# Performance work log

Measured on AMD Instinct MI355X. Metric: run time of the kernel, lower is better.

## Reference

```python
import jax, jax.numpy as jnp
import numpy as np

N_NODES = 100000
N_HEDGES = 30000
N_PINS = 400000
D = 128          # hidden_channels
H = 4            # heads
K = D // H       # per-head dim
N_BLOCKS = 4     # n_layers=2, each layer = (vertex2edge, edge2vertex)
LN_EPS = 1e-5


def setup_inputs() -> dict:
    key = jax.random.key(0)
    ks = jax.random.split(key, 10)
    s = 1.0 / np.sqrt(D)
    return {
        "x_0": jax.random.normal(ks[0], (N_NODES, D), jnp.float32),
        "Kw": jax.random.normal(ks[1], (N_BLOCKS, H, D, K), jnp.float32) * s,
        "Vw": jax.random.normal(ks[2], (N_BLOCKS, H, D, K), jnp.float32) * s,
        "Qw": jax.random.normal(ks[3], (N_BLOCKS, H, K), jnp.float32) * s,
        "W1": jax.random.normal(ks[4], (N_BLOCKS, D, D), jnp.float32) * s,
        "b1": jnp.zeros((N_BLOCKS, D), jnp.float32),
        "W2": jax.random.normal(ks[5], (N_BLOCKS, D, D), jnp.float32) * s,
        "b2": jnp.zeros((N_BLOCKS, D), jnp.float32),
        "ln0_g": jnp.ones((N_BLOCKS, D), jnp.float32),
        "ln0_b": jnp.zeros((N_BLOCKS, D), jnp.float32),
        "ln1_g": jnp.ones((N_BLOCKS, D), jnp.float32),
        "ln1_b": jnp.zeros((N_BLOCKS, D), jnp.float32),
        "node_idx": jax.random.randint(ks[6], (N_PINS,), 0, N_NODES),
        "hedge_idx": jax.random.randint(ks[7], (N_PINS,), 0, N_HEDGES),
        "n_hyperedges": N_HEDGES,
    }


def _ln(x, g, b):
    mu = jnp.mean(x, -1, keepdims=True)
    var = jnp.mean((x - mu) ** 2, -1, keepdims=True)
    return (x - mu) * jax.lax.rsqrt(var + LN_EPS) * g + b


def _segment_softmax(logits, seg, num_segments):
    # softmax over incident pins grouped by target (sparse softmax over source dim)
    m = jax.ops.segment_max(logits, seg, num_segments=num_segments)
    ex = jnp.exp(logits - m[seg])
    denom = jax.ops.segment_sum(ex, seg, num_segments=num_segments)
    return ex / denom[seg]


def _block(x_src, src, tgt, n_tgt, Kw, Vw, Qw, W1, b1, W2, b2, g0, be0, g1, be1):
    # Multi-head PMA attention with a single learned query per head.
    Kx = jnp.einsum('nd,hdk->nhk', x_src, Kw)           # [n_src, H, K]
    Vx = jnp.einsum('nd,hdk->nhk', x_src, Vw)           # [n_src, H, K]
    logits = jnp.einsum('hk,nhk->nh', Qw, Kx)           # [n_src, H]
    w = _segment_softmax(logits[src], tgt, n_tgt)       # [E, H]
    msg = (w[:, :, None] * Vx[src]).reshape(-1, H * K)  # [E, D] head-concat
    agg = jax.ops.segment_sum(msg, tgt, num_segments=n_tgt)  # [n_tgt, D]
    x = _ln(agg + Qw.reshape(1, H * K), g0, be0)        # Q skip + LN0
    h = jnp.maximum(x @ W1 + b1, 0.0) @ W2 + b2         # 2-layer MLP
    return _ln(x + h, g1, be1)                          # residual + LN1


def reference(x_0, Kw, Vw, Qw, W1, b1, W2, b2, ln0_g, ln0_b, ln1_g, ln1_b,
              node_idx, hedge_idx, n_hyperedges):
    n_nodes = x_0.shape[0]
    x0, x1 = x_0, None
    for layer in range(N_BLOCKS // 2):
        bv, bev = 2 * layer, 2 * layer + 1
        # vertex -> hyperedge
        x1 = jax.nn.relu(_block(x0, node_idx, hedge_idx, n_hyperedges,
                                Kw[bv], Vw[bv], Qw[bv], W1[bv], b1[bv], W2[bv], b2[bv],
                                ln0_g[bv], ln0_b[bv], ln1_g[bv], ln1_b[bv]))
        # hyperedge -> vertex
        x0 = jax.nn.relu(_block(x1, hedge_idx, node_idx, n_nodes,
                                Kw[bev], Vw[bev], Qw[bev], W1[bev], b1[bev], W2[bev], b2[bev],
                                ln0_g[bev], ln0_b[bev], ln1_g[bev], ln1_b[bev]))
    return (x0, x1)
```

## Files before the change

### kernel.cpp

```cpp
#include <hip/hip_runtime.h>

#define N_NODES 100000
#define N_HEDGES 30000
#define N_PINS 400000
#define NPN 100096
#define NPH 30080
#define OVF_CAP 8192
#define SCAN_BH 118
#define SCAN_BN 391

typedef __attribute__((ext_vector_type(8))) short bf16x8;
typedef __attribute__((ext_vector_type(4))) float f32x4;
typedef unsigned short ushort_t;

__device__ __forceinline__ unsigned short f2bf(float f) {
  unsigned int u = __float_as_uint(f);
  u += 0x7FFF + ((u >> 16) & 1);
  return (unsigned short)(u >> 16);
}
__device__ __forceinline__ float bf2f(unsigned short s) {
  return __uint_as_float(((unsigned int)s) << 16);
}
__device__ __forceinline__ void gload16(const void* g, void* l) {
  __builtin_amdgcn_global_load_lds(
      (const __attribute__((address_space(1))) unsigned int*)g,
      (__attribute__((address_space(3))) unsigned int*)l, 16, 0, 0);
}

__global__ __launch_bounds__(256) void fused_front(
    const float* __restrict__ x0_in, ushort_t* __restrict__ x0b,
    const int* __restrict__ node_idx, const int* __restrict__ hedge_idx,
    int* __restrict__ cntN, int* __restrict__ cntH, unsigned* __restrict__ rank2,
    const float* __restrict__ Kw, const float* __restrict__ Vw,
    const float* __restrict__ Qw, const float* __restrict__ W1,
    const float* __restrict__ W2, ushort_t* __restrict__ Vvqsw,
    ushort_t* __restrict__ W1sw, ushort_t* __restrict__ W2sw) {
  int gsz = gridDim.x * 256;
  int tid = blockIdx.x * 256 + threadIdx.x;
  int rn = 0, rh = 0;
  bool hasPin = tid < N_PINS;
  if (hasPin) {
    int n_i = node_idx[tid], h_i = hedge_idx[tid];
    rn = atomicAdd(&cntN[n_i], 1);
    rh = atomicAdd(&cntH[h_i], 1);
  }
  for (int i = tid; i < N_NODES * 16; i += gsz) {
    const float4* s = (const float4*)x0_in + (size_t)i * 2;
    float4 a = s[0], b = s[1];
    uint4 o;
    o.x = ((unsigned)f2bf(a.y) << 16) | f2bf(a.x);
    o.y = ((unsigned)f2bf(a.w) << 16) | f2bf(a.z);
    o.z = ((unsigned)f2bf(b.y) << 16) | f2bf(b.x);
    o.w = ((unsigned)f2bf(b.w) << 16) | f2bf(b.z);
    ((uint4*)x0b)[i] = o;
  }
  for (int i = tid; i < 4 * 144 * 128; i += gsz) {
    int b = i / 18432, r = i % 18432, c = r >> 7, d = r & 127;
    float v;
    if (c < 128) {
      v = Vw[((b * 4 + (c >> 5)) * 128 + d) * 32 + (c & 31)];
    } else if (c < 132) {
      int h = c - 128;
      const float* kp = Kw + ((b * 4 + h) * 128 + d) * 32;
      const float* qp = Qw + (b * 4 + h) * 32;
      float s = 0.f;
      for (int k = 0; k < 32; ++k) s += kp[k] * qp[k];
      v = s;
    } else {
      v = 0.f;
    }
    int L = (c * 256 + d * 2) ^ ((c & 7) << 4);
    Vvqsw[b * 18432 + L / 2] = f2bf(v);
  }
  for (int i = tid; i < 4 * 128 * 128; i += gsz) {
    int b = i >> 14, r = i & 16383, c = r >> 7, k = r & 127;
    int L = (c * 256 + k * 2) ^ ((c & 7) << 4);
    int idx = b * 16384 + L / 2;
    W1sw[idx] = f2bf(W1[b * 16384 + k * 128 + c]);
    W2sw[idx] = f2bf(W2[b * 16384 + k * 128 + c]);
  }
  if (hasPin) rank2[tid] = ((unsigned)rh << 16) | (unsigned)rn;
}

__global__ __launch_bounds__(256) void csr_scan2(
    const int* __restrict__ cntH, int2* __restrict__ segH, int* __restrict__ ovfH,
    const int* __restrict__ cntN, int2* __restrict__ segN, int* __restrict__ ovfN,
    int* __restrict__ gctr) {
  __shared__ int wsum[4];
  __shared__ int bbase;
  bool isH = (int)blockIdx.x < SCAN_BH;
  const int* cnt = isH ? cntH : cntN;
  int2* seg = isH ? segH : segN;
  int* ovf = isH ? ovfH : ovfN;
  int* g = gctr + (isH ? 0 : 1);
  int* oc = gctr + (isH ? 2 : 3);
  int thresh = isH ? 32 : 16;
  int n = isH ? N_HEDGES : N_NODES;
  int i = (isH ? (int)blockIdx.x : (int)blockIdx.x - SCAN_BH) * 256 + threadIdx.x;
  int lane = threadIdx.x & 63, wid = threadIdx.x >> 6;
  int v = (i < n) ? cnt[i] : 0;
  int sc = v;
#pragma unroll
  for (int s = 1; s < 64; s <<= 1) {
    int tv = __shfl_up(sc, s);
    if (lane >= s) sc += tv;
  }
  if (lane == 63) wsum[wid] = sc;
  __syncthreads();
  if (threadIdx.x == 0) {
    int s0 = wsum[0], s1 = wsum[1], s2 = wsum[2], s3 = wsum[3];
    wsum[0] = 0; wsum[1] = s0; wsum[2] = s0 + s1; wsum[3] = s0 + s1 + s2;
    bbase = atomicAdd(g, s0 + s1 + s2 + s3);
  }
  __syncthreads();
  if (i < n) {
    int st = bbase + wsum[wid] + (sc - v);
    seg[i] = make_int2(st, v);
    if (v > thresh) {
      int k = atomicAdd(oc, 1);
      if (k < OVF_CAP) ovf[k] = i;
    }
  }
}

__global__ __launch_bounds__(256) void csr_fill(
    const int* __restrict__ node_idx, const int* __restrict__ hedge_idx,
    const unsigned* __restrict__ rank2, const int2* __restrict__ segN,
    const int2* __restrict__ segH, int* __restrict__ pinsN,
    int* __restrict__ pinsH) {
  int e = blockIdx.x * 256 + threadIdx.x;
  if (e < N_PINS) {
    int n = node_idx[e], h = hedge_idx[e];
    unsigned r2 = rank2[e];
    pinsH[segH[h].x + (int)(r2 >> 16)] = n;
    pinsN[segN[n].x + (int)(r2 & 0xffffu)] = h;
  }
}

__global__ __launch_bounds__(256) void transform_k(
    const ushort_t* __restrict__ xb, const ushort_t* __restrict__ Bsw,
    ushort_t* __restrict__ Vxb, float* __restrict__ lg, int n) {
  __shared__ char Blds[36864];
  __shared__ char Olds[16384];
  int t = threadIdx.x, l = t & 63, w = t >> 6;
  size_t r0 = (size_t)blockIdx.x * 64;
#pragma unroll
  for (int it = 0; it < 9; ++it) {
    int off = it * 4096 + w * 1024 + l * 16;
    gload16((const char*)Bsw + off, Blds + off);
  }
  __syncthreads();

  f32x4 acc[9];
#pragma unroll
  for (int ct = 0; ct < 9; ++ct) acc[ct] = (f32x4){0.f, 0.f, 0.f, 0.f};
  int swz = (l & 7) << 4;
  int lbase = (l & 15) * 256 + (l >> 4) * 16;
  const ushort_t* abase = xb + (r0 + w * 16 + (l & 15)) * 128 + (l >> 4) * 8;
#pragma unroll
  for (int kk = 0; kk < 4; ++kk) {
    bf16x8 a = *(const bf16x8*)(abase + kk * 32);
#pragma unroll
    for (int ct = 0; ct < 9; ++ct) {
      bf16x8 b = *(const bf16x8*)(Blds + ((ct * 4096 + kk * 64 + lbase) ^ swz));
      acc[ct] = __builtin_amdgcn_mfma_f32_16x16x32_bf16(a, b, acc[ct], 0, 0, 0);
    }
  }
  if ((l & 15) < 4) {
    size_t rb = r0 + w * 16 + (l >> 4) * 4;
#pragma unroll
    for (int j = 0; j < 4; ++j) lg[(rb + j) * 4 + (l & 15)] = acc[8][j];
  }
  int row64 = w * 16 + (l >> 4) * 4;
#pragma unroll
  for (int ct = 0; ct < 8; ++ct) {
    int c2 = (ct * 16 + (l & 15)) * 2;
#pragma unroll
    for (int j = 0; j < 4; ++j) {
      int r = row64 + j;
      int addr = (r * 256 + c2) ^ ((r & 0xC) << 3);
      *(ushort_t*)(Olds + addr) = f2bf(acc[ct][j]);
    }
  }
  __syncthreads();
#pragma unroll
  for (int it = 0; it < 4; ++it) {
    int L = it * 4096 + t * 16;
    int r = L >> 8;
    int phys = L ^ ((r & 0xC) << 3);
    *(uint4*)((char*)Vxb + r0 * 256 + L) = *(const uint4*)(Olds + phys);
  }
}

template <int L>
__global__ __launch_bounds__(256) void attn_g(
    const ushort_t* __restrict__ Vxb, const float* __restrict__ lg,
    const int2* __restrict__ seg, const int* __restrict__ pins,
    const float* __restrict__ Qflat, const float* __restrict__ g0,
    const float* __restrict__ be0, ushort_t* __restrict__ xmidb, int n_tgt,
    int mainBlocks, const int* __restrict__ ovf, const int* __restrict__ ovfcnt) {
  constexpr int G = 64 / L;
  constexpr int C = 128 / L;
  __shared__ float wl[4][G][L][4];
  __shared__ int pl[4][G][L];
  int wid = threadIdx.x >> 6, lane = threadIdx.x & 63;
  const char* vb = (const char*)Vxb;

  if ((int)blockIdx.x < mainBlocks) {
    int g = lane / L, li = lane % L;
    int tg = ((int)blockIdx.x * 4 + wid) * G + g;
    bool tval = tg < n_tgt;
    int2 sc = tval ? seg[tg] : make_int2(0, 0);
    int base = sc.x, deg = sc.y;
    bool fast = deg <= L;
    int mydeg = (tval && fast) ? deg : 0;
    bool act = li < mydeg;
    int p = act ? pins[base + li] : 0;
    float4 l4;
    if (act) l4 = *(const float4*)(lg + p * 4);
    else l4 = make_float4(-3.4e38f, -3.4e38f, -3.4e38f, -3.4e38f);
    float m0 = l4.x, m1 = l4.y, m2 = l4.z, m3 = l4.w;
#pragma unroll
    for (int off = 1; off < L; off <<= 1) {
      m0 = fmaxf(m0, __shfl_xor(m0, off));
      m1 = fmaxf(m1, __shfl_xor(m1, off));
      m2 = fmaxf(m2, __shfl_xor(m2, off));
      m3 = fmaxf(m3, __shfl_xor(m3, off));
    }
    float e0 = __expf(l4.x - m0), e1 = __expf(l4.y - m1);
    float e2 = __expf(l4.z - m2), e3 = __expf(l4.w - m3);
    float s0 = e0, s1 = e1, s2 = e2, s3 = e3;
#pragma unroll
    for (int off = 1; off < L; off <<= 1) {
      s0 += __shfl_xor(s0, off);
      s1 += __shfl_xor(s1, off);
      s2 += __shfl_xor(s2, off);
      s3 += __shfl_xor(s3, off);
    }
    wl[wid][g][li][0] = e0 / s0;
    wl[wid][g][li][1] = e1 / s1;
    wl[wid][g][li][2] = e2 / s2;
    wl[wid][g][li][3] = e3 / s3;
    pl[wid][g][li] = p << 8;

    int myh = li / (L / 4);
    float acc[C];
#pragma unroll
    for (int c = 0; c < C; ++c) acc[c] = 0.f;
    for (int e = 0; e < mydeg; ++e) {
      int off = pl[wid][g][e];
      float wgt = wl[wid][g][e][myh];
      const char* src = vb + off + li * (C * 2);
      unsigned u[C / 2];
      if constexpr (C == 8) {
        uint4 v = *(const uint4*)src;
        u[0] = v.x; u[1] = v.y; u[2] = v.z; u[3] = v.w;
      } else {
        uint2 v = *(const uint2*)src;
        u[0] = v.x; u[1] = v.y;
      }
#pragma unroll
      for (int j = 0; j < C / 2; ++j) {
        acc[2 * j] = fmaf(wgt, __uint_as_float(u[j] << 16), acc[2 * j]);
        acc[2 * j + 1] = fmaf(wgt, __uint_as_float(u[j] & 0xffff0000u), acc[2 * j + 1]);
      }
    }
    float q[C], gv[C], bv[C];
#pragma unroll
    for (int j = 0; j < C / 4; ++j) {
      float4 t = *(const float4*)(Qflat + li * C + j * 4);
      q[j * 4] = t.x; q[j * 4 + 1] = t.y; q[j * 4 + 2] = t.z; q[j * 4 + 3] = t.w;
      t = *(const float4*)(g0 + li * C + j * 4);
      gv[j * 4] = t.x; gv[j * 4 + 1] = t.y; gv[j * 4 + 2] = t.z; gv[j * 4 + 3] = t.w;
      t = *(const float4*)(be0 + li * C + j * 4);
      bv[j * 4] = t.x; bv[j * 4 + 1] = t.y; bv[j * 4 + 2] = t.z; bv[j * 4 + 3] = t.w;
    }
    float t1 = 0.f, t2 = 0.f;
#pragma unroll
    for (int c = 0; c < C; ++c) {
      float x = acc[c] + q[c];
      acc[c] = x;
      t1 += x;
      t2 += x * x;
    }
#pragma unroll
    for (int off = 1; off < L; off <<= 1) {
      t1 += __shfl_xor(t1, off);
      t2 += __shfl_xor(t2, off);
    }
    float mean = t1 * (1.f / 128.f);
    float var = t2 * (1.f / 128.f) - mean * mean;
    float rs = rsqrtf(var + 1e-5f);
    if (tval && fast) {
      float o[C];
#pragma unroll
      for (int c = 0; c < C; ++c) o[c] = (acc[c] - mean) * rs * gv[c] + bv[c];
      char* dst = (char*)xmidb + (size_t)tg * 256 + li * (C * 2);
      if constexpr (C == 8) {
        uint4 pk;
        pk.x = ((unsigned)f2bf(o[1]) << 16) | f2bf(o[0]);
        pk.y = ((unsigned)f2bf(o[3]) << 16) | f2bf(o[2]);
        pk.z = ((unsigned)f2bf(o[5]) << 16) | f2bf(o[4]);
        pk.w = ((unsigned)f2bf(o[7]) << 16) | f2bf(o[6]);
        *(uint4*)dst = pk;
      } else {
        uint2 pk;
        pk.x = ((unsigned)f2bf(o[1]) << 16) | f2bf(o[0]);
        pk.y = ((unsigned)f2bf(o[3]) << 16) | f2bf(o[2]);
        *(uint2*)dst = pk;
      }
    }
    return;
  }

  int cnt = *ovfcnt;
  if (cnt > OVF_CAP) cnt = OVF_CAP;
  int head = lane >> 4;
  for (int idx = ((int)blockIdx.x - mainBlocks) * 4 + wid; idx < cnt; idx += 128) {
    int tg = ovf[idx];
    int2 sc = seg[tg];
    int base = sc.x, deg = sc.y;
    float m0 = -3.4e38f, m1 = -3.4e38f, m2 = -3.4e38f, m3 = -3.4e38f;
    for (int i = lane; i < deg; i += 64) {
      int p = pins[base + i];
      float4 l4 = *(const float4*)(lg + p * 4);
      m0 = fmaxf(m0, l4.x); m1 = fmaxf(m1, l4.y);
      m2 = fmaxf(m2, l4.z); m3 = fmaxf(m3, l4.w);
    }
#pragma unroll
    for (int off = 1; off < 64; off <<= 1) {
      m0 = fmaxf(m0, __shfl_xor(m0, off));
      m1 = fmaxf(m1, __shfl_xor(m1, off));
      m2 = fmaxf(m2, __shfl_xor(m2, off));
      m3 = fmaxf(m3, __shfl_xor(m3, off));
    }
    float s0 = 0.f, s1 = 0.f, s2 = 0.f, s3 = 0.f;
    for (int i = lane; i < deg; i += 64) {
      int p = pins[base + i];
      float4 l4 = *(const float4*)(lg + p * 4);
      s0 += __expf(l4.x - m0); s1 += __expf(l4.y - m1);
      s2 += __expf(l4.z - m2); s3 += __expf(l4.w - m3);
    }
#pragma unroll
    for (int off = 1; off < 64; off <<= 1) {
      s0 += __shfl_xor(s0, off);
      s1 += __shfl_xor(s1, off);
      s2 += __shfl_xor(s2, off);
      s3 += __shfl_xor(s3, off);
    }
    float mh = (head & 2) ? ((head & 1) ? m3 : m2) : ((head & 1) ? m1 : m0);
    float sh = (head & 2) ? ((head & 1) ? s3 : s2) : ((head & 1) ? s1 : s0);
    float rdh = (deg > 0) ? 1.f / sh : 0.f;
    float acc0 = 0.f, acc1 = 0.f;
    for (int e = 0; e < deg; ++e) {
      int p = pins[base + e];
      float w0 = __expf(lg[p * 4 + head] - mh) * rdh;
      unsigned int v = *(const unsigned int*)(vb + (p << 8) + lane * 4);
      acc0 = fmaf(w0, __uint_as_float(v << 16), acc0);
      acc1 = fmaf(w0, __uint_as_float(v & 0xffff0000u), acc1);
    }
    float2 q2 = ((const float2*)Qflat)[lane];
    float x0v = acc0 + q2.x;
    float x1v = acc1 + q2.y;
    float t1 = x0v + x1v, t2 = x0v * x0v + x1v * x1v;
#pragma unroll
    for (int off = 1; off < 64; off <<= 1) {
      t1 += __shfl_xor(t1, off);
      t2 += __shfl_xor(t2, off);
    }
    float mean = t1 * (1.f / 128.f);
    float var = t2 * (1.f / 128.f) - mean * mean;
    float rs = rsqrtf(var + 1e-5f);
    float2 gg = ((const float2*)g0)[lane];
    float2 bb = ((const float2*)be0)[lane];
    float o0 = (x0v - mean) * rs * gg.x + bb.x;
    float o1 = (x1v - mean) * rs * gg.y + bb.y;
    unsigned int pk = ((unsigned int)f2bf(o1) << 16) | f2bf(o0);
    ((unsigned int*)xmidb)[tg * 64 + lane] = pk;
  }
}

__global__ __launch_bounds__(256) void mlp_k(
    const ushort_t* __restrict__ xmb, const ushort_t* __restrict__ W1sw,
    const float* __restrict__ b1, const ushort_t* __restrict__ W2sw,
    const float* __restrict__ b2, const float* __restrict__ g1,
    const float* __restrict__ be1, float* __restrict__ outf,
    ushort_t* __restrict__ outb, int n, int flags) {
  __shared__ char Wlds[32768];
  __shared__ char Hlds[16384];
  int t = threadIdx.x, l = t & 63, w = t >> 6;
  size_t r0 = (size_t)blockIdx.x * 64;
#pragma unroll
  for (int it = 0; it < 8; ++it) {
    int off = it * 4096 + w * 1024 + l * 16;
    gload16((const char*)W1sw + off, Wlds + off);
  }
  float b1v[8], b2v[8], g1v[8], be1v[8];
#pragma unroll
  for (int ct = 0; ct < 8; ++ct) {
    int c = ct * 16 + (l & 15);
    b1v[ct] = b1[c]; b2v[ct] = b2[c]; g1v[ct] = g1[c]; be1v[ct] = be1[c];
  }
  __syncthreads();

  int swz = (l & 7) << 4;
  int lbase = (l & 15) * 256 + (l >> 4) * 16;
  f32x4 acc[8];
#pragma unroll
  for (int ct = 0; ct < 8; ++ct) acc[ct] = (f32x4){b1v[ct], b1v[ct], b1v[ct], b1v[ct]};
  const ushort_t* abase = xmb + (r0 + w * 16 + (l & 15)) * 128 + (l >> 4) * 8;
#pragma unroll
  for (int kk = 0; kk < 4; ++kk) {
    bf16x8 a = *(const bf16x8*)(abase + kk * 32);
#pragma unroll
    for (int ct = 0; ct < 8; ++ct) {
      bf16x8 b = *(const bf16x8*)(Wlds + ((ct * 4096 + kk * 64 + lbase) ^ swz));
      acc[ct] = __builtin_amdgcn_mfma_f32_16x16x32_bf16(a, b, acc[ct], 0, 0, 0);
    }
  }
  int hbase = w * 4096;
#pragma unroll
  for (int ct = 0; ct < 8; ++ct) {
    int c2 = (ct * 16 + (l & 15)) * 2;
#pragma unroll
    for (int j = 0; j < 4; ++j) {
      int rl = (l >> 4) * 4 + j;
      int addr = hbase + ((rl * 256 + c2) ^ ((rl & 7) << 4));
      *(ushort_t*)(Hlds + addr) = f2bf(fmaxf(acc[ct][j], 0.f));
    }
  }
  __syncthreads();
#pragma unroll
  for (int it = 0; it < 8; ++it) {
    int off = it * 4096 + w * 1024 + l * 16;
    gload16((const char*)W2sw + off, Wlds + off);
  }
  __syncthreads();

  f32x4 acc2[8];
#pragma unroll
  for (int ct = 0; ct < 8; ++ct) acc2[ct] = (f32x4){b2v[ct], b2v[ct], b2v[ct], b2v[ct]};
#pragma unroll
  for (int kk = 0; kk < 4; ++kk) {
    bf16x8 a = *(const bf16x8*)(Hlds + (hbase + ((lbase + kk * 64) ^ swz)));
#pragma unroll
    for (int ct = 0; ct < 8; ++ct) {
      bf16x8 b = *(const bf16x8*)(Wlds + ((ct * 4096 + kk * 64 + lbase) ^ swz));
      acc2[ct] = __builtin_amdgcn_mfma_f32_16x16x32_bf16(a, b, acc2[ct], 0, 0, 0);
    }
  }
  size_t rbase = r0 + w * 16 + (l >> 4) * 4;
  float s1[4] = {0.f, 0.f, 0.f, 0.f}, s2[4] = {0.f, 0.f, 0.f, 0.f};
#pragma unroll
  for (int ct = 0; ct < 8; ++ct) {
    int c = ct * 16 + (l & 15);
#pragma unroll
    for (int j = 0; j < 4; ++j) {
      float x = bf2f(xmb[(rbase + j) * 128 + c]);
      float y = acc2[ct][j] + x;
      acc2[ct][j] = y;
      s1[j] += y;
      s2[j] += y * y;
    }
  }
#pragma unroll
  for (int off = 1; off < 16; off <<= 1) {
#pragma unroll
    for (int j = 0; j < 4; ++j) {
      s1[j] += __shfl_xor(s1[j], off);
      s2[j] += __shfl_xor(s2[j], off);
    }
  }
  float mean[4], rs[4];
#pragma unroll
  for (int j = 0; j < 4; ++j) {
    mean[j] = s1[j] * (1.f / 128.f);
    float var = s2[j] * (1.f / 128.f) - mean[j] * mean[j];
    rs[j] = rsqrtf(var + 1e-5f);
  }
#pragma unroll
  for (int ct = 0; ct < 8; ++ct) {
    int c = ct * 16 + (l & 15);
#pragma unroll
    for (int j = 0; j < 4; ++j) {
      float o = fmaxf((acc2[ct][j] - mean[j]) * rs[j] * g1v[ct] + be1v[ct], 0.f);
      size_t row = rbase + j;
      if (flags & 2) outb[row * 128 + c] = f2bf(o);
      if ((flags & 1) && row < (size_t)n) outf[row * 128 + c] = o;
    }
  }
}

extern "C" void kernel_launch(void* const* d_in, const int* in_sizes, int n_in,
                              void* d_out, int out_size, void* d_ws, size_t ws_size,
                              hipStream_t stream) {
  const float* x0_in = (const float*)d_in[0];
  const float* Kw  = (const float*)d_in[1];
  const float* Vw  = (const float*)d_in[2];
  const float* Qw  = (const float*)d_in[3];
  const float* W1  = (const float*)d_in[4];
  const float* b1  = (const float*)d_in[5];
  const float* W2  = (const float*)d_in[6];
  const float* b2  = (const float*)d_in[7];
  const float* ln0g = (const float*)d_in[8];
  const float* ln0b = (const float*)d_in[9];
  const float* ln1g = (const float*)d_in[10];
  const float* ln1b = (const float*)d_in[11];
  const int* node_idx  = (const int*)d_in[12];
  const int* hedge_idx = (const int*)d_in[13];

  float* out = (float*)d_out;
  float* x0_out = out;
  float* x1_out = out + (size_t)N_NODES * 128;

  char* w = (char*)d_ws;
  auto alloc = [&](size_t bytes) -> void* {
    void* p = (void*)w;
    w += (bytes + 255) & ~(size_t)255;
    return p;
  };
  ushort_t* Vvqsw = (ushort_t*)alloc(4 * 18432 * 2);
  ushort_t* W1sw  = (ushort_t*)alloc(4 * 16384 * 2);
  ushort_t* W2sw  = (ushort_t*)alloc(4 * 16384 * 2);
  ushort_t* x0b   = (ushort_t*)alloc((size_t)NPN * 128 * 2);
  ushort_t* x1b   = (ushort_t*)alloc((size_t)NPH * 128 * 2);
  ushort_t* Vxb   = (ushort_t*)alloc((size_t)NPN * 128 * 2);
  float*    lg    = (float*)alloc((size_t)NPN * 4 * 4);
  ushort_t* xmidb = (ushort_t*)alloc((size_t)NPN * 128 * 2);
  int2* segH  = (int2*)alloc((size_t)N_HEDGES * 8);
  int2* segN  = (int2*)alloc((size_t)N_NODES * 8);
  int* pinsH  = (int*)alloc(N_PINS * 4);
  int* pinsN  = (int*)alloc(N_PINS * 4);
  int* ovfH   = (int*)alloc(OVF_CAP * 4);
  int* ovfN   = (int*)alloc(OVF_CAP * 4);
  unsigned* rank2 = (unsigned*)alloc((size_t)N_PINS * 4);
  int* zbase  = (int*)alloc((size_t)(N_HEDGES + N_NODES + 4) * 4);
  int* cntH = zbase;
  int* cntN = cntH + N_HEDGES;
  int* gctr = cntN + N_NODES;

  hipMemsetAsync(zbase, 0, (size_t)(N_HEDGES + N_NODES + 4) * 4, stream);

  fused_front<<<2048, 256, 0, stream>>>(x0_in, x0b, node_idx, hedge_idx, cntN, cntH,
                                        rank2, Kw, Vw, Qw, W1, W2, Vvqsw, W1sw, W2sw);
  csr_scan2<<<SCAN_BH + SCAN_BN, 256, 0, stream>>>(cntH, segH, ovfH,
                                                   cntN, segN, ovfN, gctr);
  csr_fill<<<(N_PINS + 255) / 256, 256, 0, stream>>>(node_idx, hedge_idx, rank2,
                                                     segN, segH, pinsN, pinsH);

  const ushort_t* srcs[4] = {x0b, x1b, x0b, x1b};
  int n_srcs[4] = {N_NODES, N_HEDGES, N_NODES, N_HEDGES};
  const int2* segs[4] = {segH, segN, segH, segN};
  const int* pinss[4] = {pinsH, pinsN, pinsH, pinsN};
  int n_tgts[4] = {N_HEDGES, N_NODES, N_HEDGES, N_NODES};
  float* outf[4] = {x1_out, x0_out, x1_out, x0_out};
  ushort_t* outbs[4] = {x1b, x0b, x1b, x0b};
  int flags[4] = {2, 2, 3, 1};

  const int mbH = (N_HEDGES + 7) / 8;
  const int mbN = (N_NODES + 15) / 16;

  for (int b = 0; b < 4; ++b) {
    int n_src = n_srcs[b], n_tgt = n_tgts[b];
    transform_k<<<(n_src + 63) / 64, 256, 0, stream>>>(srcs[b], Vvqsw + b * 18432,
                                                       Vxb, lg, n_src);
    if (b & 1) {
      attn_g<16><<<mbN + 32, 256, 0, stream>>>(Vxb, lg, segs[b], pinss[b],
                                               Qw + b * 128, ln0g + b * 128,
                                               ln0b + b * 128, xmidb, n_tgt,
                                               mbN, ovfN, gctr + 3);
    } else {
      attn_g<32><<<mbH + 32, 256, 0, stream>>>(Vxb, lg, segs[b], pinss[b],
                                               Qw + b * 128, ln0g + b * 128,
                                               ln0b + b * 128, xmidb, n_tgt,
                                               mbH, ovfH, gctr + 2);
    }
    mlp_k<<<(n_tgt + 63) / 64, 256, 0, stream>>>(xmidb, W1sw + b * 16384, b1 + b * 128,
                                                 W2sw + b * 16384, b2 + b * 128,
                                                 ln1g + b * 128, ln1b + b * 128,
                                                 outf[b], outbs[b], n_tgt, flags[b]);
  }
}
```

Before: 287.8 us.

## Fuse block-0 V/logit transform into the front kernel and skip its launch

The front kernel now also computes the first block's V projection and attention logits directly from the fp32 input, building the swizzled bf16 weight tile in LDS per workgroup and running MFMA on 64 rows per block. The separate transform launch for block 0 is skipped, which removes one kernel launch and one re-read of the bf16-converted x0. In exchange, every workgroup redundantly builds the 144x128 weight tile (including K·Q dot products), and the grid shrinks to 1563 blocks with 36KB of LDS each, which may lower occupancy for the atomic and conversion parts of the kernel.

```diff
diff --git a/kernel.cpp b/kernel.cpp
--- a/kernel.cpp
+++ b/kernel.cpp
@@ -8,6 +8,7 @@
 #define OVF_CAP 8192
 #define SCAN_BH 118
 #define SCAN_BN 391
+#define FRONT_BLOCKS 1563
 
 typedef __attribute__((ext_vector_type(8))) short bf16x8;
 typedef __attribute__((ext_vector_type(4))) float f32x4;
@@ -26,17 +27,29 @@
       (const __attribute__((address_space(1))) unsigned int*)g,
       (__attribute__((address_space(3))) unsigned int*)l, 16, 0, 0);
 }
-
-__global__ __launch_bounds__(256) void fused_front(
+__device__ __forceinline__ bf16x8 pack8(float4 a0, float4 a1) {
+  bf16x8 r;
+  r[0] = (short)f2bf(a0.x); r[1] = (short)f2bf(a0.y);
+  r[2] = (short)f2bf(a0.z); r[3] = (short)f2bf(a0.w);
+  r[4] = (short)f2bf(a1.x); r[5] = (short)f2bf(a1.y);
+  r[6] = (short)f2bf(a1.z); r[7] = (short)f2bf(a1.w);
+  return r;
+}
+
+__global__ __launch_bounds__(256) void front2(
     const float* __restrict__ x0_in, ushort_t* __restrict__ x0b,
     const int* __restrict__ node_idx, const int* __restrict__ hedge_idx,
     int* __restrict__ cntN, int* __restrict__ cntH, unsigned* __restrict__ rank2,
     const float* __restrict__ Kw, const float* __restrict__ Vw,
     const float* __restrict__ Qw, const float* __restrict__ W1,
     const float* __restrict__ W2, ushort_t* __restrict__ Vvqsw,
-    ushort_t* __restrict__ W1sw, ushort_t* __restrict__ W2sw) {
+    ushort_t* __restrict__ W1sw, ushort_t* __restrict__ W2sw,
+    ushort_t* __restrict__ Vxb, float* __restrict__ lg) {
+  __shared__ char Blds[36864];
   int gsz = gridDim.x * 256;
   int tid = blockIdx.x * 256 + threadIdx.x;
+  int t = threadIdx.x, l = t & 63, w = t >> 6;
+
   int rn = 0, rh = 0;
   bool hasPin = tid < N_PINS;
   if (hasPin) {
@@ -44,6 +57,74 @@
     rn = atomicAdd(&cntN[n_i], 1);
     rh = atomicAdd(&cntH[h_i], 1);
   }
+
+  for (int i = t; i < 144 * 128; i += 256) {
+    int c = i >> 7, d = i & 127;
+    float v;
+    if (c < 128) {
+      v = Vw[((c >> 5) * 128 + d) * 32 + (c & 31)];
+    } else if (c < 132) {
+      int h = c - 128;
+      const float* kp = Kw + (h * 128 + d) * 32;
+      const float* qp = Qw + h * 32;
+      float s = 0.f;
+      for (int k = 0; k < 32; ++k) s += kp[k] * qp[k];
+      v = s;
+    } else {
+      v = 0.f;
+    }
+    int L = (c * 256 + d * 2) ^ ((c & 7) << 4);
+    *(ushort_t*)(Blds + L) = f2bf(v);
+  }
+  __syncthreads();
+
+  f32x4 acc[9];
+#pragma unroll
+  for (int ct = 0; ct < 9; ++ct) acc[ct] = (f32x4){0.f, 0.f, 0.f, 0.f};
+  int swz = (l & 7) << 4;
+  int lbase = (l & 15) * 256 + (l >> 4) * 16;
+  size_t r0 = (size_t)blockIdx.x * 64;
+  size_t arow = r0 + w * 16 + (l & 15);
+  if (arow > (size_t)(N_NODES - 1)) arow = N_NODES - 1;
+  const float* ap = x0_in + arow * 128 + (l >> 4) * 8;
+#pragma unroll
+  for (int kk = 0; kk < 4; ++kk) {
+    float4 a0 = *(const float4*)(ap + kk * 32);
+    float4 a1 = *(const float4*)(ap + kk * 32 + 4);
+    bf16x8 a = pack8(a0, a1);
+#pragma unroll
+    for (int ct = 0; ct < 9; ++ct) {
+      bf16x8 b = *(const bf16x8*)(Blds + ((ct * 4096 + kk * 64 + lbase) ^ swz));
+      acc[ct] = __builtin_amdgcn_mfma_f32_16x16x32_bf16(a, b, acc[ct], 0, 0, 0);
+    }
+  }
+  if ((l & 15) < 4) {
+    size_t rb = r0 + w * 16 + (l >> 4) * 4;
+#pragma unroll
+    for (int j = 0; j < 4; ++j) lg[(rb + j) * 4 + (l & 15)] = acc[8][j];
+  }
+  __syncthreads();
+  char* Olds = Blds;
+  int row64 = w * 16 + (l >> 4) * 4;
+#pragma unroll
+  for (int ct = 0; ct < 8; ++ct) {
+    int c2 = (ct * 16 + (l & 15)) * 2;
+#pragma unroll
+    for (int j = 0; j < 4; ++j) {
+      int r = row64 + j;
+      int addr = (r * 256 + c2) ^ ((r & 0xC) << 3);
+      *(ushort_t*)(Olds + addr) = f2bf(acc[ct][j]);
+    }
+  }
+  __syncthreads();
+#pragma unroll
+  for (int it = 0; it < 4; ++it) {
+    int L = it * 4096 + t * 16;
+    int r = L >> 8;
+    int phys = L ^ ((r & 0xC) << 3);
+    *(uint4*)((char*)Vxb + r0 * 256 + L) = *(const uint4*)(Olds + phys);
+  }
+
   for (int i = tid; i < N_NODES * 16; i += gsz) {
     const float4* s = (const float4*)x0_in + (size_t)i * 2;
     float4 a = s[0], b = s[1];
@@ -541,8 +622,9 @@
 
   hipMemsetAsync(zbase, 0, (size_t)(N_HEDGES + N_NODES + 4) * 4, stream);
 
-  fused_front<<<2048, 256, 0, stream>>>(x0_in, x0b, node_idx, hedge_idx, cntN, cntH,
-                                        rank2, Kw, Vw, Qw, W1, W2, Vvqsw, W1sw, W2sw);
+  front2<<<FRONT_BLOCKS, 256, 0, stream>>>(
+      x0_in, x0b, node_idx, hedge_idx, cntN, cntH, rank2,
+      Kw, Vw, Qw, W1, W2, Vvqsw, W1sw, W2sw, Vxb, lg);
   csr_scan2<<<SCAN_BH + SCAN_BN, 256, 0, stream>>>(cntH, segH, ovfH,
                                                    cntN, segN, ovfN, gctr);
   csr_fill<<<(N_PINS + 255) / 256, 256, 0, stream>>>(node_idx, hedge_idx, rank2,
@@ -562,8 +644,10 @@
 
   for (int b = 0; b < 4; ++b) {
     int n_src = n_srcs[b], n_tgt = n_tgts[b];
-    transform_k<<<(n_src + 63) / 64, 256, 0, stream>>>(srcs[b], Vvqsw + b * 18432,
-                                                       Vxb, lg, n_src);
+    if (b > 0) {
+      transform_k<<<(n_src + 63) / 64, 256, 0, stream>>>(srcs[b], Vvqsw + b * 18432,
+                                                         Vxb, lg, n_src);
+    }
     if (b & 1) {
       attn_g<16><<<mbN + 32, 256, 0, stream>>>(Vxb, lg, segs[b], pinss[b],
                                                Qw + b * 128, ln0g + b * 128,
```

Measured after the change: 345.3 us. 1.2x slower.

## Fuse next block's V/logit transform into MLP epilogue

Applied to the files above, without the earlier changes.

The MLP kernel for blocks 0-2 now keeps its bf16 output tile in shared memory and immediately multiplies it by the next block's V/Q weight matrix, writing Vxb and the logits directly. This drops the separate transform_k launches and the bf16 round-trip of x0b/x1b between kernels. The cost is 64KB of LDS per block, which may reduce occupancy, plus extra MFMA work and syncs inside the MLP kernel.

```diff
diff --git a/kernel.cpp b/kernel.cpp
--- a/kernel.cpp
+++ b/kernel.cpp
@@ -380,14 +380,17 @@
   }
 }
 
-__global__ __launch_bounds__(256) void mlp_k(
+__global__ __launch_bounds__(256) void mlp_tf(
     const ushort_t* __restrict__ xmb, const ushort_t* __restrict__ W1sw,
     const float* __restrict__ b1, const ushort_t* __restrict__ W2sw,
     const float* __restrict__ b2, const float* __restrict__ g1,
-    const float* __restrict__ be1, float* __restrict__ outf,
-    ushort_t* __restrict__ outb, int n, int flags) {
-  __shared__ char Wlds[32768];
-  __shared__ char Hlds[16384];
+    const float* __restrict__ be1, float* __restrict__ outf, int n, int wf32,
+    const ushort_t* __restrict__ Bsw, ushort_t* __restrict__ Vxb,
+    float* __restrict__ lg) {
+  __shared__ char S[65536];
+  char* Wlds = S;
+  char* Hlds = S + 32768;
+  char* Xout = S + 49152;
   int t = threadIdx.x, l = t & 63, w = t >> 6;
   size_t r0 = (size_t)blockIdx.x * 64;
 #pragma unroll
@@ -405,6 +408,7 @@
 
   int swz = (l & 7) << 4;
   int lbase = (l & 15) * 256 + (l >> 4) * 16;
+  int hbase = w * 4096;
   f32x4 acc[8];
 #pragma unroll
   for (int ct = 0; ct < 8; ++ct) acc[ct] = (f32x4){b1v[ct], b1v[ct], b1v[ct], b1v[ct]};
@@ -418,7 +422,6 @@
       acc[ct] = __builtin_amdgcn_mfma_f32_16x16x32_bf16(a, b, acc[ct], 0, 0, 0);
     }
   }
-  int hbase = w * 4096;
 #pragma unroll
   for (int ct = 0; ct < 8; ++ct) {
     int c2 = (ct * 16 + (l & 15)) * 2;
@@ -481,12 +484,172 @@
 #pragma unroll
   for (int ct = 0; ct < 8; ++ct) {
     int c = ct * 16 + (l & 15);
+    int c2 = c * 2;
+#pragma unroll
+    for (int j = 0; j < 4; ++j) {
+      float o = fmaxf((acc2[ct][j] - mean[j]) * rs[j] * g1v[ct] + be1v[ct], 0.f);
+      int rl = (l >> 4) * 4 + j;
+      int addr = hbase + ((rl * 256 + c2) ^ ((rl & 7) << 4));
+      *(ushort_t*)(Xout + addr) = f2bf(o);
+      size_t row = rbase + j;
+      if (wf32 && row < (size_t)n) outf[row * 128 + c] = o;
+    }
+  }
+  __syncthreads();
+
+  char* Blds = S;
+#pragma unroll
+  for (int it = 0; it < 9; ++it) {
+    int off = it * 4096 + w * 1024 + l * 16;
+    gload16((const char*)Bsw + off, Blds + off);
+  }
+  __syncthreads();
+
+  f32x4 ta[9];
+#pragma unroll
+  for (int ct = 0; ct < 9; ++ct) ta[ct] = (f32x4){0.f, 0.f, 0.f, 0.f};
+#pragma unroll
+  for (int kk = 0; kk < 4; ++kk) {
+    bf16x8 a = *(const bf16x8*)(Xout + (hbase + ((lbase + kk * 64) ^ swz)));
+#pragma unroll
+    for (int ct = 0; ct < 9; ++ct) {
+      bf16x8 b = *(const bf16x8*)(Blds + ((ct * 4096 + kk * 64 + lbase) ^ swz));
+      ta[ct] = __builtin_amdgcn_mfma_f32_16x16x32_bf16(a, b, ta[ct], 0, 0, 0);
+    }
+  }
+  if ((l & 15) < 4) {
+    size_t rb = r0 + w * 16 + (l >> 4) * 4;
+#pragma unroll
+    for (int j = 0; j < 4; ++j) lg[(rb + j) * 4 + (l & 15)] = ta[8][j];
+  }
+  __syncthreads();
+  char* Olds = Xout;
+  int row64 = w * 16 + (l >> 4) * 4;
+#pragma unroll
+  for (int ct = 0; ct < 8; ++ct) {
+    int c2 = (ct * 16 + (l & 15)) * 2;
+#pragma unroll
+    for (int j = 0; j < 4; ++j) {
+      int r = row64 + j;
+      int addr = (r * 256 + c2) ^ ((r & 0xC) << 3);
+      *(ushort_t*)(Olds + addr) = f2bf(ta[ct][j]);
+    }
+  }
+  __syncthreads();
+#pragma unroll
+  for (int it = 0; it < 4; ++it) {
+    int L = it * 4096 + t * 16;
+    int r = L >> 8;
+    int phys = L ^ ((r & 0xC) << 3);
+    *(uint4*)((char*)Vxb + r0 * 256 + L) = *(const uint4*)(Olds + phys);
+  }
+}
+
+__global__ __launch_bounds__(256) void mlp_k(
+    const ushort_t* __restrict__ xmb, const ushort_t* __restrict__ W1sw,
+    const float* __restrict__ b1, const ushort_t* __restrict__ W2sw,
+    const float* __restrict__ b2, const float* __restrict__ g1,
+    const float* __restrict__ be1, float* __restrict__ outf, int n) {
+  __shared__ char Wlds[32768];
+  __shared__ char Hlds[16384];
+  int t = threadIdx.x, l = t & 63, w = t >> 6;
+  size_t r0 = (size_t)blockIdx.x * 64;
+#pragma unroll
+  for (int it = 0; it < 8; ++it) {
+    int off = it * 4096 + w * 1024 + l * 16;
+    gload16((const char*)W1sw + off, Wlds + off);
+  }
+  float b1v[8], b2v[8], g1v[8], be1v[8];
+#pragma unroll
+  for (int ct = 0; ct < 8; ++ct) {
+    int c = ct * 16 + (l & 15);
+    b1v[ct] = b1[c]; b2v[ct] = b2[c]; g1v[ct] = g1[c]; be1v[ct] = be1[c];
+  }
+  __syncthreads();
+
+  int swz = (l & 7) << 4;
+  int lbase = (l & 15) * 256 + (l >> 4) * 16;
+  f32x4 acc[8];
+#pragma unroll
+  for (int ct = 0; ct < 8; ++ct) acc[ct] = (f32x4){b1v[ct], b1v[ct], b1v[ct], b1v[ct]};
+  const ushort_t* abase = xmb + (r0 + w * 16 + (l & 15)) * 128 + (l >> 4) * 8;
+#pragma unroll
+  for (int kk = 0; kk < 4; ++kk) {
+    bf16x8 a = *(const bf16x8*)(abase + kk * 32);
+#pragma unroll
+    for (int ct = 0; ct < 8; ++ct) {
+      bf16x8 b = *(const bf16x8*)(Wlds + ((ct * 4096 + kk * 64 + lbase) ^ swz));
+      acc[ct] = __builtin_amdgcn_mfma_f32_16x16x32_bf16(a, b, acc[ct], 0, 0, 0);
+    }
+  }
+  int hbase = w * 4096;
+#pragma unroll
+  for (int ct = 0; ct < 8; ++ct) {
+    int c2 = (ct * 16 + (l & 15)) * 2;
+#pragma unroll
+    for (int j = 0; j < 4; ++j) {
+      int rl = (l >> 4) * 4 + j;
+      int addr = hbase + ((rl * 256 + c2) ^ ((rl & 7) << 4));
+      *(ushort_t*)(Hlds + addr) = f2bf(fmaxf(acc[ct][j], 0.f));
+    }
+  }
+  __syncthreads();
+#pragma unroll
+  for (int it = 0; it < 8; ++it) {
+    int off = it * 4096 + w * 1024 + l * 16;
+    gload16((const char*)W2sw + off, Wlds + off);
+  }
+  __syncthreads();
+
+  f32x4 acc2[8];
+#pragma unroll
+  for (int ct = 0; ct < 8; ++ct) acc2[ct] = (f32x4){b2v[ct], b2v[ct], b2v[ct], b2v[ct]};
+#pragma unroll
+  for (int kk = 0; kk < 4; ++kk) {
+    bf16x8 a = *(const bf16x8*)(Hlds + (hbase + ((lbase + kk * 64) ^ swz)));
+#pragma unroll
+    for (int ct = 0; ct < 8; ++ct) {
+      bf16x8 b = *(const bf16x8*)(Wlds + ((ct * 4096 + kk * 64 + lbase) ^ swz));
+      acc2[ct] = __builtin_amdgcn_mfma_f32_16x16x32_bf16(a, b, acc2[ct], 0, 0, 0);
+    }
+  }
+  size_t rbase = r0 + w * 16 + (l >> 4) * 4;
+  float s1[4] = {0.f, 0.f, 0.f, 0.f}, s2[4] = {0.f, 0.f, 0.f, 0.f};
+#pragma unroll
+  for (int ct = 0; ct < 8; ++ct) {
+    int c = ct * 16 + (l & 15);
+#pragma unroll
+    for (int j = 0; j < 4; ++j) {
+      float x = bf2f(xmb[(rbase + j) * 128 + c]);
+      float y = acc2[ct][j] + x;
+      acc2[ct][j] = y;
+      s1[j] += y;
+      s2[j] += y * y;
+    }
+  }
+#pragma unroll
+  for (int off = 1; off < 16; off <<= 1) {
+#pragma unroll
+    for (int j = 0; j < 4; ++j) {
+      s1[j] += __shfl_xor(s1[j], off);
+      s2[j] += __shfl_xor(s2[j], off);
+    }
+  }
+  float mean[4], rs[4];
+#pragma unroll
+  for (int j = 0; j < 4; ++j) {
+    mean[j] = s1[j] * (1.f / 128.f);
+    float var = s2[j] * (1.f / 128.f) - mean[j] * mean[j];
+    rs[j] = rsqrtf(var + 1e-5f);
+  }
+#pragma unroll
+  for (int ct = 0; ct < 8; ++ct) {
+    int c = ct * 16 + (l & 15);
 #pragma unroll
     for (int j = 0; j < 4; ++j) {
       float o = fmaxf((acc2[ct][j] - mean[j]) * rs[j] * g1v[ct] + be1v[ct], 0.f);
       size_t row = rbase + j;
-      if (flags & 2) outb[row * 128 + c] = f2bf(o);
-      if ((flags & 1) && row < (size_t)n) outf[row * 128 + c] = o;
+      if (row < (size_t)n) outf[row * 128 + c] = o;
     }
   }
 }
@@ -523,7 +686,6 @@
   ushort_t* W1sw  = (ushort_t*)alloc(4 * 16384 * 2);
   ushort_t* W2sw  = (ushort_t*)alloc(4 * 16384 * 2);
   ushort_t* x0b   = (ushort_t*)alloc((size_t)NPN * 128 * 2);
-  ushort_t* x1b   = (ushort_t*)alloc((size_t)NPH * 128 * 2);
   ushort_t* Vxb   = (ushort_t*)alloc((size_t)NPN * 128 * 2);
   float*    lg    = (float*)alloc((size_t)NPN * 4 * 4);
   ushort_t* xmidb = (ushort_t*)alloc((size_t)NPN * 128 * 2);
@@ -548,22 +710,16 @@
   csr_fill<<<(N_PINS + 255) / 256, 256, 0, stream>>>(node_idx, hedge_idx, rank2,
                                                      segN, segH, pinsN, pinsH);
 
-  const ushort_t* srcs[4] = {x0b, x1b, x0b, x1b};
-  int n_srcs[4] = {N_NODES, N_HEDGES, N_NODES, N_HEDGES};
   const int2* segs[4] = {segH, segN, segH, segN};
   const int* pinss[4] = {pinsH, pinsN, pinsH, pinsN};
   int n_tgts[4] = {N_HEDGES, N_NODES, N_HEDGES, N_NODES};
-  float* outf[4] = {x1_out, x0_out, x1_out, x0_out};
-  ushort_t* outbs[4] = {x1b, x0b, x1b, x0b};
-  int flags[4] = {2, 2, 3, 1};
-
   const int mbH = (N_HEDGES + 7) / 8;
   const int mbN = (N_NODES + 15) / 16;
 
+  transform_k<<<(N_NODES + 63) / 64, 256, 0, stream>>>(x0b, Vvqsw, Vxb, lg, N_NODES);
+
   for (int b = 0; b < 4; ++b) {
-    int n_src = n_srcs[b], n_tgt = n_tgts[b];
-    transform_k<<<(n_src + 63) / 64, 256, 0, stream>>>(srcs[b], Vvqsw + b * 18432,
-                                                       Vxb, lg, n_src);
+    int n_tgt = n_tgts[b];
     if (b & 1) {
       attn_g<16><<<mbN + 32, 256, 0, stream>>>(Vxb, lg, segs[b], pinss[b],
                                                Qw + b * 128, ln0g + b * 128,
@@ -575,9 +731,17 @@
                                                ln0b + b * 128, xmidb, n_tgt,
                                                mbH, ovfH, gctr + 2);
     }
-    mlp_k<<<(n_tgt + 63) / 64, 256, 0, stream>>>(xmidb, W1sw + b * 16384, b1 + b * 128,
-                                                 W2sw + b * 16384, b2 + b * 128,
-                                                 ln1g + b * 128, ln1b + b * 128,
-                                                 outf[b], outbs[b], n_tgt, flags[b]);
-  }
-}
+    if (b < 3) {
+      int wf32 = (b == 2) ? 1 : 0;
+      float* of = (b == 2) ? x1_out : nullptr;
+      mlp_tf<<<(n_tgt + 63) / 64, 256, 0, stream>>>(
+          xmidb, W1sw + b * 16384, b1 + b * 128, W2sw + b * 16384, b2 + b * 128,
+          ln1g + b * 128, ln1b + b * 128, of, n_tgt, wf32,
+          Vvqsw + (b + 1) * 18432, Vxb, lg);
+    } else {
+      mlp_k<<<(n_tgt + 63) / 64, 256, 0, stream>>>(
+          xmidb, W1sw + b * 16384, b1 + b * 128, W2sw + b * 16384, b2 + b * 128,
+          ln1g + b * 128, ln1b + b * 128, x0_out, n_tgt);
+    }
+  }
+}
```

After: 269.3 us. 6.4% less time.
